# Optimization experiments

Hardware: AMD Instinct MI355X
Metric: run time of the kernel (lower is better)

## Reference

```python
import jax, jax.numpy as jnp
import numpy as np
import math

D_MODEL = 1024
NUM_HEADS = 16
HEAD_DIM = D_MODEL // NUM_HEADS
THETA = 10000.0
B, S = 2, 2048


def _rope(x, positions, theta):
    # x: (b, h, s, d); positions: (s,) int
    d = x.shape[-1]
    inv_freq = theta ** (-jnp.arange(0, d, 2, dtype=jnp.float32) / d)  # (d/2,)
    ang = positions.astype(jnp.float32)[:, None] * inv_freq[None, :]   # (s, d/2)
    cos, sin = jnp.cos(ang), jnp.sin(ang)
    x1 = x[..., ::2]
    x2 = x[..., 1::2]
    r1 = x1 * cos - x2 * sin
    r2 = x1 * sin + x2 * cos
    # interleave back to (..., d)
    return jnp.stack([r1, r2], axis=-1).reshape(x.shape)


def setup_inputs() -> dict:
    key = jax.random.key(0)
    ks = jax.random.split(key, 5)
    std = math.sqrt(2.0 / (D_MODEL + D_MODEL))
    return {
        "x": jax.random.normal(ks[0], (B, S, D_MODEL), dtype=jnp.float32),
        "token_positions": jnp.arange(S, dtype=jnp.int32),
        "Wq": jax.random.normal(ks[1], (D_MODEL, D_MODEL), dtype=jnp.float32) * std,
        "Wk": jax.random.normal(ks[2], (D_MODEL, D_MODEL), dtype=jnp.float32) * std,
        "Wv": jax.random.normal(ks[3], (D_MODEL, D_MODEL), dtype=jnp.float32) * std,
        "Wo": jax.random.normal(ks[4], (D_MODEL, D_MODEL), dtype=jnp.float32) * std,
    }


def reference(x, token_positions, Wq, Wk, Wv, Wo):
    b, s, _ = x.shape
    def split_heads(t):
        return t.reshape(b, s, NUM_HEADS, HEAD_DIM).transpose(0, 2, 1, 3)  # (b,h,s,d)
    Q = split_heads(x @ Wq.T)
    K = split_heads(x @ Wk.T)
    V = split_heads(x @ Wv.T)
    Q = _rope(Q, token_positions, THETA)
    K = _rope(K, token_positions, THETA)
    scores = jnp.einsum("bhqd,bhkd->bhqk", Q, K) / math.sqrt(HEAD_DIM)
    causal = jnp.tril(jnp.ones((s, s), dtype=bool))
    scores = jnp.where(causal, scores, -jnp.inf)
    attn = jax.nn.softmax(scores, axis=-1)
    out = jnp.einsum("bhqk,bhkd->bhqd", attn, V)
    out = out.transpose(0, 2, 1, 3).reshape(b, s, D_MODEL)
    return out @ Wo.T
```

## Files before the change

kernel.cpp:

```cpp
#include <hip/hip_runtime.h>
#include <math.h>

typedef unsigned short u16;
typedef unsigned int   u32;
typedef __attribute__((ext_vector_type(8))) short bf16x8;
typedef __attribute__((ext_vector_type(4))) float floatx4;
typedef __attribute__((ext_vector_type(4))) _Float16 halfx4;
typedef __attribute__((ext_vector_type(2))) unsigned int uintx2;

#define SEQ 2048
#define DM  1024
#define NH  16
#define DH  64
#define MM  4096
#define QSCALE 0.18033688011112042f

__device__ __forceinline__ u16 f2bf(float f) {
    u32 u = __builtin_bit_cast(u32, f);
    u += 0x7fffu + ((u >> 16) & 1u);
    return (u16)(u >> 16);
}

__device__ __forceinline__ void async16(const void* g, void* l) {
    __builtin_amdgcn_global_load_lds(
        (const __attribute__((address_space(1))) void*)g,
        (__attribute__((address_space(3))) void*)l, 16, 0, 0);
}

__global__ __launch_bounds__(256) void cvt_shuf(const float* __restrict__ x,
                                                const float* __restrict__ w0,
                                                const float* __restrict__ w1,
                                                const float* __restrict__ w2,
                                                const float* __restrict__ w3,
                                                u16* __restrict__ Xsh,
                                                u16* __restrict__ Wsh) {
    const int bid = blockIdx.x, cb = blockIdx.y, tid = threadIdx.x;
    const float* src; u16* dst; int row0;
    if (bid < 64) { src = x; dst = Xsh; row0 = bid * 64; }
    else {
        int wi = (bid - 64) >> 4;
        src = (wi == 0) ? w0 : (wi == 1) ? w1 : (wi == 2) ? w2 : w3;
        dst = Wsh + (size_t)wi * DM * DM;
        row0 = ((bid - 64) & 15) * 64;
    }
    __shared__ __align__(16) u16 t[64 * 64];
#pragma unroll
    for (int rep = 0; rep < 4; ++rep) {
        int f = rep * 256 + tid;
        int r = f >> 4, c4 = f & 15;
        float4 v = *(const float4*)&src[(size_t)(row0 + r) * DM + cb * 64 + c4 * 4];
        uint2 pk;
        pk.x = (u32)f2bf(v.x) | ((u32)f2bf(v.y) << 16);
        pk.y = (u32)f2bf(v.z) | ((u32)f2bf(v.w) << 16);
        int ch = (c4 >> 1) ^ (r & 7);
        *(uint2*)&t[r * 64 + ch * 8 + (c4 & 1) * 4] = pk;
    }
    __syncthreads();
#pragma unroll
    for (int rep = 0; rep < 2; ++rep) {
        int s = rep * 256 + tid;
        int tile = s >> 6, l = s & 63;
        int mt = tile >> 1, kt = tile & 1, lm = l & 15, quad = l >> 4;
        int m = mt * 16 + lm;
        uint4 v = *(const uint4*)&t[m * 64 + ((kt * 4 + quad) ^ (m & 7)) * 8];
        size_t rowblk = (size_t)(row0 >> 4) + mt;
        size_t ktile  = cb * 2 + kt;
        *(uint4*)&dst[(rowblk * 32 + ktile) * 512 + l * 8] = v;
    }
}

__global__ void rope_tab_kernel(const int* __restrict__ pos, float2* __restrict__ tab) {
    int i = blockIdx.x * 256 + threadIdx.x;
    int p = i >> 5, d2 = i & 31;
    float freq = __expf(-(float)d2 * (9.2103403719761836f / 32.0f));
    float sv, cv;
    sincosf((float)pos[p] * freq, &sv, &cv);
    tab[i] = make_float2(cv, sv);
}

__global__ __launch_bounds__(256) void transpose_v(const u16* __restrict__ V, _Float16* __restrict__ Vt) {
    const int s0 = blockIdx.x * 64;
    const int b = blockIdx.y >> 4, h = blockIdx.y & 15;
    const int tid = threadIdx.x;
    __shared__ __align__(16) u16 t[64 * 72];
#pragma unroll
    for (int rep = 0; rep < 2; ++rep) {
        int f = rep * 256 + tid;
        int row = f >> 3, cc = (f & 7) * 8;
        *(uint4*)&t[row * 72 + cc] =
            *(const uint4*)&V[(size_t)(b * SEQ + s0 + row) * DM + h * DH + cc];
    }
    __syncthreads();
#pragma unroll
    for (int rep = 0; rep < 2; ++rep) {
        int f = rep * 256 + tid;
        int drow = f >> 3, cc = (f & 7) * 8;
        _Float16 o[8];
#pragma unroll
        for (int j = 0; j < 8; ++j) {
            u32 bits = (u32)t[(cc + j) * 72 + drow] << 16;
            o[j] = (_Float16)__builtin_bit_cast(float, bits);
        }
        *(uint4*)&Vt[(size_t)((b * NH + h) * DH + drow) * SEQ + s0 + cc] = *(uint4*)o;
    }
}

template<int NT, bool OUTF32>
__global__ __launch_bounds__(256, 2) void gemm_nl(const u16* __restrict__ Ash,
                                                  const u16* __restrict__ Wbase,
                                                  u16* __restrict__ outbf,
                                                  float* __restrict__ outf,
                                                  const float2* __restrict__ ropetab,
                                                  int ropeMask) {
    const int z  = blockIdx.z;
    const u16* Wp = Wbase + (size_t)z * (DM * DM);
    const int m0 = blockIdx.x * 64, n0 = blockIdx.y * (NT * 64);
    const int tid  = threadIdx.x;
    const int lane = tid & 63, w = tid >> 6;
    const int lm = lane & 15, quad = lane >> 4;

    const u16* aB = Ash + ((size_t)(m0 >> 4) * 32) * 512 + lane * 8;
    const u16* bB = Wp  + ((size_t)((n0 >> 4) + w * NT) * 32) * 512 + lane * 8;

    floatx4 acc[4][NT];
    const floatx4 z4 = {0.f, 0.f, 0.f, 0.f};
#pragma unroll
    for (int mt = 0; mt < 4; ++mt)
#pragma unroll
        for (int nt = 0; nt < NT; ++nt) acc[mt][nt] = z4;

    bf16x8 ca[2][4], cb2[2][NT];
#pragma unroll
    for (int ks = 0; ks < 2; ++ks) {
#pragma unroll
        for (int mt = 0; mt < 4; ++mt)
            ca[ks][mt] = *(const bf16x8*)(aB + (size_t)mt * 16384 + ks * 512);
#pragma unroll
        for (int nt = 0; nt < NT; ++nt)
            cb2[ks][nt] = *(const bf16x8*)(bB + (size_t)nt * 16384 + ks * 512);
    }

#pragma unroll 2
    for (int it = 0; it < 16; ++it) {
        bf16x8 na[2][4], nb[2][NT];
        if (it < 15) {
            const size_t ko = (size_t)(it + 1) * 1024;
#pragma unroll
            for (int ks = 0; ks < 2; ++ks) {
#pragma unroll
                for (int mt = 0; mt < 4; ++mt)
                    na[ks][mt] = *(const bf16x8*)(aB + (size_t)mt * 16384 + ko + ks * 512);
#pragma unroll
                for (int nt = 0; nt < NT; ++nt)
                    nb[ks][nt] = *(const bf16x8*)(bB + (size_t)nt * 16384 + ko + ks * 512);
            }
        }
#pragma unroll
        for (int ks = 0; ks < 2; ++ks)
#pragma unroll
            for (int mt = 0; mt < 4; ++mt)
#pragma unroll
                for (int nt = 0; nt < NT; ++nt)
                    acc[mt][nt] = __builtin_amdgcn_mfma_f32_16x16x32_bf16(ca[ks][mt], cb2[ks][nt], acc[mt][nt], 0, 0, 0);
        if (it < 15) {
#pragma unroll
            for (int ks = 0; ks < 2; ++ks) {
#pragma unroll
                for (int mt = 0; mt < 4; ++mt) ca[ks][mt] = na[ks][mt];
#pragma unroll
                for (int nt = 0; nt < NT; ++nt) cb2[ks][nt] = nb[ks][nt];
            }
        }
    }

    const bool rope = OUTF32 ? false : (((ropeMask >> z) & 1) != 0);
    const float osc = (!OUTF32 && z == 0) ? QSCALE : 1.0f;

#pragma unroll
    for (int mt = 0; mt < 4; ++mt)
#pragma unroll
        for (int r = 0; r < 4; ++r) {
            int row = m0 + mt * 16 + quad * 4 + r;
#pragma unroll
            for (int nt = 0; nt < NT; ++nt) {
                int col = n0 + w * (NT * 16) + nt * 16 + lm;
                float v  = acc[mt][nt][r];
                if (rope) {
                    float pv = __shfl_xor(v, 1);
                    float2 cs = ropetab[(row & (SEQ - 1)) * 32 + ((col & 63) >> 1)];
                    v = (lm & 1) ? fmaf(pv, cs.y, v * cs.x) : fmaf(v, cs.x, -pv * cs.y);
                }
                v *= osc;
                if (OUTF32) {
                    outf[(size_t)row * DM + col] = v;
                } else {
                    float hv = __shfl_xor(v, 1);
                    if (!(lm & 1)) {
                        u32 pk = (u32)f2bf(v) | ((u32)f2bf(hv) << 16);
                        *(u32*)&outbf[(size_t)z * ((size_t)MM * DM) + (size_t)row * DM + col] = pk;
                    }
                }
            }
        }
}

__global__ __launch_bounds__(512) void attn_kernel(const u16* __restrict__ Q,
                                                   const u16* __restrict__ K,
                                                   const _Float16* __restrict__ Vt,
                                                   u16* __restrict__ AO) {
    const int u  = blockIdx.x;
    const int qt = (u < 256) ? (15 - (u >> 5)) : ((u >> 5) - 8);
    const int bh = u & 31;
    const int b  = bh >> 4, h = bh & 15;
    const int q0 = qt * 128;
    const int tid = threadIdx.x, w = tid >> 6, lane = tid & 63;
    const int lm = lane & 15, quad = lane >> 4;

    __shared__ __align__(16) u16      lsK[2][128 * 64];
    __shared__ __align__(16) _Float16 lsV[2][64 * 128];

    bf16x8 qb[2];
#pragma unroll
    for (int ks = 0; ks < 2; ++ks)
        qb[ks] = *(const bf16x8*)
            &Q[(size_t)(b * SEQ + q0 + w * 16 + lm) * DM + h * DH + ks * 32 + quad * 8];

    const floatx4 z4 = {0.f, 0.f, 0.f, 0.f};
    floatx4 o[4];
#pragma unroll
    for (int dt = 0; dt < 4; ++dt) o[dt] = z4;
    float lsum = 0.f;

    const int qloc = w * 16 + lm;

    auto stageKV = [&](int buf, int kt) {
#pragma unroll
        for (int rep = 0; rep < 2; ++rep) {
            int f = rep * 512 + tid;
            int krow = f >> 3, kcb = (f & 7) ^ (krow & 7);
            async16(&K[(size_t)(b * SEQ + kt * 128 + krow) * DM + h * DH + kcb * 8],
                    &lsK[buf][f * 8]);
            int d = f >> 4, gbs = (f & 15) ^ ((d >> 1) & 7);
            async16(&Vt[(size_t)(bh * DH + d) * SEQ + kt * 128 + gbs * 8],
                    &lsV[buf][f * 8]);
        }
    };

    stageKV(0, 0);
    for (int kt = 0; kt <= qt; ++kt) {
        __syncthreads();
        if (kt < qt) stageKV((kt + 1) & 1, kt + 1);
        const u16*      Lk = lsK[kt & 1];
        const _Float16* Lv = lsV[kt & 1];

        floatx4 s4[8];
#pragma unroll
        for (int st = 0; st < 8; ++st) s4[st] = z4;
#pragma unroll
        for (int ks = 0; ks < 2; ++ks) {
            const int cbl = ((ks * 4 + quad) ^ (lm & 7)) * 8;
#pragma unroll
            for (int st = 0; st < 8; ++st) {
                bf16x8 ka = *(const bf16x8*)&Lk[(st * 16 + lm) * 64 + cbl];
                s4[st] = __builtin_amdgcn_mfma_f32_16x16x32_bf16(ka, qb[ks], s4[st], 0, 0, 0);
            }
        }

        halfx4 pb[8];
        const bool diag = (kt == qt);
#pragma unroll
        for (int st = 0; st < 8; ++st) {
#pragma unroll
            for (int r = 0; r < 4; ++r) {
                float v = s4[st][r];
                if (diag) {
                    int keyloc = st * 16 + quad * 4 + r;
                    if (keyloc > qloc) v = -1e30f;
                }
                v = exp2f(v);
                lsum += v;
                s4[st][r] = v;
            }
            uintx2 pk2;
            pk2.x = __builtin_bit_cast(u32, __builtin_amdgcn_cvt_pkrtz(s4[st][0], s4[st][1]));
            pk2.y = __builtin_bit_cast(u32, __builtin_amdgcn_cvt_pkrtz(s4[st][2], s4[st][3]));
            pb[st] = __builtin_bit_cast(halfx4, pk2);
        }

#pragma unroll
        for (int st = 0; st < 8; ++st) {
#pragma unroll
            for (int dt = 0; dt < 4; ++dt) {
                int drow = dt * 16 + lm;
                int sbs = (st * 2 + (quad >> 1)) ^ ((drow >> 1) & 7);
                halfx4 va = *(const halfx4*)&Lv[drow * 128 + sbs * 8 + (quad & 1) * 4];
                o[dt] = __builtin_amdgcn_mfma_f32_16x16x16f16(va, pb[st], o[dt], 0, 0, 0);
            }
        }
    }

    lsum += __shfl_xor(lsum, 16);
    lsum += __shfl_xor(lsum, 32);
    float rl = 1.0f / lsum;

    __syncthreads();
    u16* eb = (u16*)&lsK[0][0];
    const int q = w * 16 + lm;
#pragma unroll
    for (int dt = 0; dt < 4; ++dt) {
        uint2 pk;
        pk.x = (u32)f2bf(o[dt][0] * rl) | ((u32)f2bf(o[dt][1] * rl) << 16);
        pk.y = (u32)f2bf(o[dt][2] * rl) | ((u32)f2bf(o[dt][3] * rl) << 16);
        int ch = (dt * 2 + (quad >> 1)) ^ (lm & 7);
        *(uint2*)&eb[q * 64 + ch * 8 + (quad & 1) * 4] = pk;
    }
    __syncthreads();
    const size_t rowblk = (size_t)((b * SEQ + q0) >> 4) + w;
#pragma unroll
    for (int kt = 0; kt < 2; ++kt) {
        uint4 v = *(const uint4*)&eb[(w * 16 + lm) * 64 + ((kt * 4 + quad) ^ (lm & 7)) * 8];
        *(uint4*)&AO[(rowblk * 32 + (h * 2 + kt)) * 512 + lane * 8] = v;
    }
}

extern "C" void kernel_launch(void* const* d_in, const int* in_sizes, int n_in,
                              void* d_out, int out_size, void* d_ws, size_t ws_size,
                              hipStream_t stream) {
    const float* x   = (const float*)d_in[0];
    const int*   pos = (const int*)d_in[1];
    float* out = (float*)d_out;

    u16* ws = (u16*)d_ws;
    const size_t MD = (size_t)MM * DM;
    const size_t DD = (size_t)DM * DM;
    u16* Xsh = ws;
    u16* Wsh = ws + MD;
    u16* Qbf = ws + MD + 4 * DD;
    u16* Kbf = Qbf + MD;
    u16* Vbf = Kbf + MD;
    u16* VtB = Vbf + MD;
    float2* ropetab = (float2*)(VtB + MD);
    _Float16* Vt = (_Float16*)VtB;
    u16* AOsh = Xsh;

    cvt_shuf<<<dim3(128, 16), 256, 0, stream>>>(
        x, (const float*)d_in[2], (const float*)d_in[3], (const float*)d_in[4],
        (const float*)d_in[5], Xsh, Wsh);
    rope_tab_kernel<<<SEQ * 32 / 256, 256, 0, stream>>>(pos, ropetab);

    gemm_nl<4, false><<<dim3(64, 4, 3), 256, 0, stream>>>(Xsh, Wsh, Qbf, nullptr, ropetab, 0x3);

    transpose_v<<<dim3(SEQ / 64, 2 * NH), 256, 0, stream>>>(Vbf, Vt);

    attn_kernel<<<dim3(512), 512, 0, stream>>>(Qbf, Kbf, Vt, AOsh);

    gemm_nl<2, true><<<dim3(64, 8, 1), 256, 0, stream>>>(AOsh, Wsh + 3 * DD, nullptr, out, nullptr, 0);
}
```

Baseline: 208.6 us.

## Fuse rope table into prep kernel and V transpose into QKV GEMM epilogue

Folds the rope sin/cos table computation into the conversion/shuffle kernel and removes the separate V transpose kernel. The QKV GEMM now writes V directly in transposed fp16 layout from its accumulators. It also switches the QKV GEMM to NT=2 with a larger grid and drops the min-blocks launch bound. This saves two launches and a full round trip of V through memory. In exchange the transposed stores are 8-byte strided writes, and the occupancy/tile balance changes.

```diff
diff --git a/kernel.cpp b/kernel.cpp
--- a/kernel.cpp
+++ b/kernel.cpp
@@ -27,14 +27,27 @@
         (__attribute__((address_space(3))) void*)l, 16, 0, 0);
 }
 
-__global__ __launch_bounds__(256) void cvt_shuf(const float* __restrict__ x,
-                                                const float* __restrict__ w0,
-                                                const float* __restrict__ w1,
-                                                const float* __restrict__ w2,
-                                                const float* __restrict__ w3,
-                                                u16* __restrict__ Xsh,
-                                                u16* __restrict__ Wsh) {
+__global__ __launch_bounds__(256) void prep_kernel(const float* __restrict__ x,
+                                                   const float* __restrict__ w0,
+                                                   const float* __restrict__ w1,
+                                                   const float* __restrict__ w2,
+                                                   const float* __restrict__ w3,
+                                                   u16* __restrict__ Xsh,
+                                                   u16* __restrict__ Wsh,
+                                                   const int* __restrict__ pos,
+                                                   float2* __restrict__ tab) {
     const int bid = blockIdx.x, cb = blockIdx.y, tid = threadIdx.x;
+
+    int lin = bid * 16 + cb;
+    if (lin < 256) {
+        int i = lin * 256 + tid;
+        int p = i >> 5, d2 = i & 31;
+        float freq = __expf(-(float)d2 * (9.2103403719761836f / 32.0f));
+        float sv, cv;
+        sincosf((float)pos[p] * freq, &sv, &cv);
+        tab[i] = make_float2(cv, sv);
+    }
+
     const float* src; u16* dst; int row0;
     if (bid < 64) { src = x; dst = Xsh; row0 = bid * 64; }
     else {
@@ -69,49 +82,14 @@
     }
 }
 
-__global__ void rope_tab_kernel(const int* __restrict__ pos, float2* __restrict__ tab) {
-    int i = blockIdx.x * 256 + threadIdx.x;
-    int p = i >> 5, d2 = i & 31;
-    float freq = __expf(-(float)d2 * (9.2103403719761836f / 32.0f));
-    float sv, cv;
-    sincosf((float)pos[p] * freq, &sv, &cv);
-    tab[i] = make_float2(cv, sv);
-}
-
-__global__ __launch_bounds__(256) void transpose_v(const u16* __restrict__ V, _Float16* __restrict__ Vt) {
-    const int s0 = blockIdx.x * 64;
-    const int b = blockIdx.y >> 4, h = blockIdx.y & 15;
-    const int tid = threadIdx.x;
-    __shared__ __align__(16) u16 t[64 * 72];
-#pragma unroll
-    for (int rep = 0; rep < 2; ++rep) {
-        int f = rep * 256 + tid;
-        int row = f >> 3, cc = (f & 7) * 8;
-        *(uint4*)&t[row * 72 + cc] =
-            *(const uint4*)&V[(size_t)(b * SEQ + s0 + row) * DM + h * DH + cc];
-    }
-    __syncthreads();
-#pragma unroll
-    for (int rep = 0; rep < 2; ++rep) {
-        int f = rep * 256 + tid;
-        int drow = f >> 3, cc = (f & 7) * 8;
-        _Float16 o[8];
-#pragma unroll
-        for (int j = 0; j < 8; ++j) {
-            u32 bits = (u32)t[(cc + j) * 72 + drow] << 16;
-            o[j] = (_Float16)__builtin_bit_cast(float, bits);
-        }
-        *(uint4*)&Vt[(size_t)((b * NH + h) * DH + drow) * SEQ + s0 + cc] = *(uint4*)o;
-    }
-}
-
 template<int NT, bool OUTF32>
-__global__ __launch_bounds__(256, 2) void gemm_nl(const u16* __restrict__ Ash,
-                                                  const u16* __restrict__ Wbase,
-                                                  u16* __restrict__ outbf,
-                                                  float* __restrict__ outf,
-                                                  const float2* __restrict__ ropetab,
-                                                  int ropeMask) {
+__global__ __launch_bounds__(256) void gemm_nl(const u16* __restrict__ Ash,
+                                               const u16* __restrict__ Wbase,
+                                               u16* __restrict__ outbf,
+                                               float* __restrict__ outf,
+                                               _Float16* __restrict__ vtout,
+                                               const float2* __restrict__ ropetab,
+                                               int ropeMask) {
     const int z  = blockIdx.z;
     const u16* Wp = Wbase + (size_t)z * (DM * DM);
     const int m0 = blockIdx.x * 64, n0 = blockIdx.y * (NT * 64);
@@ -171,6 +149,23 @@
                 for (int nt = 0; nt < NT; ++nt) cb2[ks][nt] = nb[ks][nt];
             }
         }
+    }
+
+    if (!OUTF32 && z == 2) {
+#pragma unroll
+        for (int mt = 0; mt < 4; ++mt) {
+            int row = m0 + mt * 16 + quad * 4;
+            int b = row >> 11, s = row & (SEQ - 1);
+#pragma unroll
+            for (int nt = 0; nt < NT; ++nt) {
+                int col = n0 + w * (NT * 16) + nt * 16 + lm;
+                uint2 pk;
+                pk.x = __builtin_bit_cast(u32, __builtin_amdgcn_cvt_pkrtz(acc[mt][nt][0], acc[mt][nt][1]));
+                pk.y = __builtin_bit_cast(u32, __builtin_amdgcn_cvt_pkrtz(acc[mt][nt][2], acc[mt][nt][3]));
+                *(uint2*)&vtout[((size_t)b * NH * DH + (size_t)col) * SEQ + s] = pk;
+            }
+        }
+        return;
     }
 
     const bool rope = OUTF32 ? false : (((ropeMask >> z) & 1) != 0);
@@ -337,22 +332,20 @@
     u16* Wsh = ws + MD;
     u16* Qbf = ws + MD + 4 * DD;
     u16* Kbf = Qbf + MD;
-    u16* Vbf = Kbf + MD;
-    u16* VtB = Vbf + MD;
+    u16* VtB = Kbf + MD;
     float2* ropetab = (float2*)(VtB + MD);
     _Float16* Vt = (_Float16*)VtB;
     u16* AOsh = Xsh;
 
-    cvt_shuf<<<dim3(128, 16), 256, 0, stream>>>(
+    prep_kernel<<<dim3(128, 16), 256, 0, stream>>>(
         x, (const float*)d_in[2], (const float*)d_in[3], (const float*)d_in[4],
-        (const float*)d_in[5], Xsh, Wsh);
-    rope_tab_kernel<<<SEQ * 32 / 256, 256, 0, stream>>>(pos, ropetab);
-
-    gemm_nl<4, false><<<dim3(64, 4, 3), 256, 0, stream>>>(Xsh, Wsh, Qbf, nullptr, ropetab, 0x3);
-
-    transpose_v<<<dim3(SEQ / 64, 2 * NH), 256, 0, stream>>>(Vbf, Vt);
+        (const float*)d_in[5], Xsh, Wsh, pos, ropetab);
+
+    gemm_nl<2, false><<<dim3(64, 8, 3), 256, 0, stream>>>(
+        Xsh, Wsh, Qbf, nullptr, Vt, ropetab, 0x3);
 
     attn_kernel<<<dim3(512), 512, 0, stream>>>(Qbf, Kbf, Vt, AOsh);
 
-    gemm_nl<2, true><<<dim3(64, 8, 1), 256, 0, stream>>>(AOsh, Wsh + 3 * DD, nullptr, out, nullptr, 0);
-}
+    gemm_nl<2, true><<<dim3(64, 8, 1), 256, 0, stream>>>(
+        AOsh, Wsh + 3 * DD, nullptr, out, nullptr, nullptr, 0);
+}
```

Result: faster. 196.2 us (-6.0%).
